# Kernel tuning notes

Hardware: AMD Instinct MI355X
Metric: run time of the kernel (lower is better)

Reference implementation:

```python
import jax, jax.numpy as jnp
import numpy as np

B, H, S, D, T = 2, 32, 8192, 128, 512


def setup_inputs() -> dict:
    key = jax.random.key(0)
    k1, k2, k3, k4 = jax.random.split(key, 4)
    return {
        "cache_k": jax.random.normal(k1, (B, H, S, D), dtype=jnp.float32),
        "cache_v": jax.random.normal(k2, (B, H, S, D), dtype=jnp.float32),
        "new_k": jax.random.normal(k3, (B, H, T, D), dtype=jnp.float32),
        "new_v": jax.random.normal(k4, (B, H, T, D), dtype=jnp.float32),
        "position_ids": jnp.arange(T, dtype=jnp.int64),  # contiguous prefill positions
    }


def reference(cache_k, cache_v, new_k, new_v, position_ids):
    # torch: cache.scatter(2, pos.expand(B,H,T,D), new) with unique positions
    # == write new_k/new_v rows into the cache along the sequence axis.
    updated_k = cache_k.at[:, :, position_ids, :].set(new_k)
    updated_v = cache_v.at[:, :, position_ids, :].set(new_v)
    return (updated_k, updated_v)
```

## Files before the change

kernel.cpp:

```cpp
#include <hip/hip_runtime.h>


#define S_LEN 8192
#define T_LEN 512
#define D_DIM 128
#define BH    64
#define ELEMS_PER_TENSOR (BH * S_LEN * D_DIM)
#define VECS_PER_BH      (S_LEN * (D_DIM / 4))
#define NEW_VECS_PER_BH  (T_LEN * (D_DIM / 4))

typedef float f4_t __attribute__((ext_vector_type(4)));

__global__ void ssc_build_map(const void* __restrict__ pos, int* __restrict__ map) {
    const int tid = threadIdx.x;
    for (int s = tid; s < S_LEN; s += 1024) map[s] = -1;
    __syncthreads();
    if (tid < T_LEN) {
        const long long* p64 = (const long long*)pos;
        const int*       p32 = (const int*)pos;
        long long a = p64[0], b = p64[1];
        bool is64 = (a >= 0) && (a < S_LEN) && (b >= 0) && (b < S_LEN) && (a != b);
        int s = is64 ? (int)p64[tid] : p32[tid];
        if (s >= 0 && s < S_LEN) map[s] = tid;
    }
}

__global__ __launch_bounds__(256) void ssc_scatter_copy(
    const f4_t* __restrict__ ck, const f4_t* __restrict__ cv,
    const f4_t* __restrict__ nk, const f4_t* __restrict__ nv,
    const int*  __restrict__ map,
    f4_t* __restrict__ ok, f4_t* __restrict__ ov) {
    const int tid = blockIdx.x * 256 + threadIdx.x;
    const int d4  = tid & 31;
    const int s   = tid >> 5;
    const int t   = map[s];

    const int bh0    = blockIdx.y * (BH / 2);
    const int dstOff = s * 32 + d4;

    if (t >= 0) {
        const int srcOff = t * 32 + d4;
        #pragma unroll 8
        for (int i = 0; i < BH / 2; ++i) {
            const int bh = bh0 + i;
            f4_t kv = __builtin_nontemporal_load(nk + srcOff + bh * NEW_VECS_PER_BH);
            f4_t vv = __builtin_nontemporal_load(nv + srcOff + bh * NEW_VECS_PER_BH);
            __builtin_nontemporal_store(kv, ok + dstOff + bh * VECS_PER_BH);
            __builtin_nontemporal_store(vv, ov + dstOff + bh * VECS_PER_BH);
        }
    } else {
        #pragma unroll 8
        for (int i = 0; i < BH / 2; ++i) {
            const int bh = bh0 + i;
            f4_t kv = __builtin_nontemporal_load(ck + dstOff + bh * VECS_PER_BH);
            f4_t vv = __builtin_nontemporal_load(cv + dstOff + bh * VECS_PER_BH);
            __builtin_nontemporal_store(kv, ok + dstOff + bh * VECS_PER_BH);
            __builtin_nontemporal_store(vv, ov + dstOff + bh * VECS_PER_BH);
        }
    }
}

extern "C" void kernel_launch(void* const* d_in, const int* in_sizes, int n_in,
                              void* d_out, int out_size, void* d_ws, size_t ws_size,
                              hipStream_t stream) {
    const f4_t* ck = (const f4_t*)d_in[0];
    const f4_t* cv = (const f4_t*)d_in[1];
    const f4_t* nk = (const f4_t*)d_in[2];
    const f4_t* nv = (const f4_t*)d_in[3];
    const void* pos = d_in[4];

    float* out = (float*)d_out;
    f4_t* ok = (f4_t*)out;
    f4_t* ov = (f4_t*)(out + ELEMS_PER_TENSOR);

    int* map = (int*)d_ws;

    ssc_build_map<<<1, 1024, 0, stream>>>(pos, map);
    ssc_scatter_copy<<<dim3(1024, 2), 256, 0, stream>>>(ck, cv, nk, nv, map, ok, ov);
}
```

Before: 227.6 us.

## Fuse position-map build into scatter copy with per-block shared-memory map

Drops the separate single-block map-building kernel. Each copy block now scans all position ids and builds an 8-entry shared-memory map for its own sequence rows. K and V are split across a new grid z dimension, so each thread streams one tensor with one unified loop and pointer increments. This removes a kernel launch and the serial dependency on a global map. In exchange every block re-reads the 512 position ids and pays two block barriers.

New measurement: 197.3 us (median of 2 runs). -13.3%, faster.

```diff
diff --git a/kernel.cpp b/kernel.cpp
--- a/kernel.cpp
+++ b/kernel.cpp
@@ -11,52 +11,57 @@
 
 typedef float f4_t __attribute__((ext_vector_type(4)));
 
-__global__ void ssc_build_map(const void* __restrict__ pos, int* __restrict__ map) {
-    const int tid = threadIdx.x;
-    for (int s = tid; s < S_LEN; s += 1024) map[s] = -1;
+__global__ __launch_bounds__(256) void ssc_fused(
+    const f4_t* __restrict__ ck, const f4_t* __restrict__ cv,
+    const f4_t* __restrict__ nk, const f4_t* __restrict__ nv,
+    const void* __restrict__ pos,
+    f4_t* __restrict__ ok, f4_t* __restrict__ ov) {
+
+    __shared__ int lmap[8];
+    const int ltid = threadIdx.x;
+    const int s0   = blockIdx.x * 8;
+
+    if (ltid < 8) lmap[ltid] = -1;
     __syncthreads();
-    if (tid < T_LEN) {
+
+    {
         const long long* p64 = (const long long*)pos;
         const int*       p32 = (const int*)pos;
         long long a = p64[0], b = p64[1];
         bool is64 = (a >= 0) && (a < S_LEN) && (b >= 0) && (b < S_LEN) && (a != b);
-        int s = is64 ? (int)p64[tid] : p32[tid];
-        if (s >= 0 && s < S_LEN) map[s] = tid;
+        #pragma unroll
+        for (int j = ltid; j < T_LEN; j += 256) {
+            int p = is64 ? (int)p64[j] : p32[j];
+            unsigned r = (unsigned)(p - s0);
+            if (r < 8u) lmap[r] = j;
+        }
     }
-}
+    __syncthreads();
 
-__global__ __launch_bounds__(256) void ssc_scatter_copy(
-    const f4_t* __restrict__ ck, const f4_t* __restrict__ cv,
-    const f4_t* __restrict__ nk, const f4_t* __restrict__ nv,
-    const int*  __restrict__ map,
-    f4_t* __restrict__ ok, f4_t* __restrict__ ov) {
-    const int tid = blockIdx.x * 256 + threadIdx.x;
+    const int tid = blockIdx.x * 256 + ltid;
     const int d4  = tid & 31;
     const int s   = tid >> 5;
-    const int t   = map[s];
+    const int t   = lmap[s & 7];
+
+    const f4_t* csrc = blockIdx.z ? cv : ck;
+    const f4_t* nsrc = blockIdx.z ? nv : nk;
+    f4_t*       odst = blockIdx.z ? ov : ok;
 
     const int bh0    = blockIdx.y * (BH / 2);
     const int dstOff = s * 32 + d4;
 
-    if (t >= 0) {
-        const int srcOff = t * 32 + d4;
-        #pragma unroll 8
-        for (int i = 0; i < BH / 2; ++i) {
-            const int bh = bh0 + i;
-            f4_t kv = __builtin_nontemporal_load(nk + srcOff + bh * NEW_VECS_PER_BH);
-            f4_t vv = __builtin_nontemporal_load(nv + srcOff + bh * NEW_VECS_PER_BH);
-            __builtin_nontemporal_store(kv, ok + dstOff + bh * VECS_PER_BH);
-            __builtin_nontemporal_store(vv, ov + dstOff + bh * VECS_PER_BH);
-        }
-    } else {
-        #pragma unroll 8
-        for (int i = 0; i < BH / 2; ++i) {
-            const int bh = bh0 + i;
-            f4_t kv = __builtin_nontemporal_load(ck + dstOff + bh * VECS_PER_BH);
-            f4_t vv = __builtin_nontemporal_load(cv + dstOff + bh * VECS_PER_BH);
-            __builtin_nontemporal_store(kv, ok + dstOff + bh * VECS_PER_BH);
-            __builtin_nontemporal_store(vv, ov + dstOff + bh * VECS_PER_BH);
-        }
+    const f4_t* src;
+    int sstride;
+    if (t >= 0) { src = nsrc + (t * 32 + d4) + bh0 * NEW_VECS_PER_BH; sstride = NEW_VECS_PER_BH; }
+    else        { src = csrc + dstOff          + bh0 * VECS_PER_BH;    sstride = VECS_PER_BH; }
+    f4_t* dst = odst + dstOff + bh0 * VECS_PER_BH;
+
+    #pragma unroll 4
+    for (int i = 0; i < BH / 2; ++i) {
+        f4_t v = __builtin_nontemporal_load(src);
+        __builtin_nontemporal_store(v, dst);
+        src += sstride;
+        dst += VECS_PER_BH;
     }
 }
 
@@ -73,8 +78,5 @@
     f4_t* ok = (f4_t*)out;
     f4_t* ov = (f4_t*)(out + ELEMS_PER_TENSOR);
 
-    int* map = (int*)d_ws;
-
-    ssc_build_map<<<1, 1024, 0, stream>>>(pos, map);
-    ssc_scatter_copy<<<dim3(1024, 2), 256, 0, stream>>>(ck, cv, nk, nv, map, ok, ov);
+    ssc_fused<<<dim3(1024, 2, 2), 256, 0, stream>>>(ck, cv, nk, nv, pos, ok, ov);
 }
```
